# Kernel optimization log

Hardware: AMD Instinct MI355X
Metric: run time of the kernel (lower is better)

The kernel has to match this reference:

```python
import jax, jax.numpy as jnp
import numpy as np

# Quantization constants (from init_kwargs)
INPUT_SCALE = 0.05
OUTPUT_SCALE = 0.1
OUTPUT_ZERO_POINT = 0
FEATURE_BITWIDTH = 8
Q_MIN = -(1 << (FEATURE_BITWIDTH - 1))       # -128
Q_MAX = (1 << (FEATURE_BITWIDTH - 1)) - 1    #  127

B, IN_F, OUT_F = 8192, 4096, 4096


def setup_inputs() -> dict:
    key = jax.random.key(0)
    k_x, k_w, k_b, k_s = jax.random.split(key, 4)
    # int8 quantized activations and weights
    x = jax.random.randint(k_x, (B, IN_F), Q_MIN, Q_MAX + 1, dtype=jnp.int8)
    weight = jax.random.randint(k_w, (OUT_F, IN_F), Q_MIN, Q_MAX + 1, dtype=jnp.int8)
    # shifted quantized bias (int32)
    bias = jax.random.randint(k_b, (OUT_F,), -1000, 1000, dtype=jnp.int32)
    # per-output-channel weight scale (positive floats)
    weight_scale = jax.random.uniform(k_s, (OUT_F,), dtype=jnp.float32, minval=0.001, maxval=0.01)
    return {"x": x, "weight": weight, "bias": bias, "weight_scale": weight_scale}


def reference(x, weight, bias, weight_scale):
    # int32-accumulated GEMM: [B, in] @ [in, out] + bias -> [B, out]
    acc = jnp.matmul(x.astype(jnp.int32), weight.astype(jnp.int32).T,
                     preferred_element_type=jnp.int32) + bias[None, :]
    # dequant/requant epilogue with per-channel scale
    out = acc.astype(jnp.float32) * (INPUT_SCALE * weight_scale[None, :] / OUTPUT_SCALE) + OUTPUT_ZERO_POINT
    out = jnp.clip(jnp.round(out), Q_MIN, Q_MAX).astype(jnp.int8)
    return out
```

## Files before the change

### kernel.cpp

```cpp
#include <hip/hip_runtime.h>
#include <cstdint>
#include <cstddef>

#define M_DIM 8192
#define N_DIM 4096
#define K_DIM 4096

#define BM 128
#define BN 128
#define BK 128

using i32x4 = __attribute__((ext_vector_type(4))) int;

__device__ __forceinline__ void async_load16(const void* g, void* l) {
    __builtin_amdgcn_global_load_lds(
        (const __attribute__((address_space(1))) void*)g,
        (__attribute__((address_space(3))) void*)l,
        16, 0, 0);
}

__global__ __launch_bounds__(256) void pack_i8_fused_kernel(const int4* __restrict__ xsrc,
                                                            const int4* __restrict__ wsrc,
                                                            unsigned* __restrict__ xdst,
                                                            unsigned* __restrict__ wdst,
                                                            long nx4, long ntot4) {
    long i = (long)blockIdx.x * blockDim.x + threadIdx.x;
    if (i >= ntot4) return;
    const int4* src;
    unsigned* dst;
    long si;
    if (i < nx4) { src = xsrc; dst = xdst; si = i; }
    else         { src = wsrc; dst = wdst; si = i - nx4; }
    int4 a = src[si];
    dst[si] = (unsigned)((a.x & 0xff) | ((a.y & 0xff) << 8) |
                         ((a.z & 0xff) << 16) | (a.w << 24));
}

__global__ __launch_bounds__(256) void qgemm_i8_kernel(const int8_t* __restrict__ A,
                                                       const int8_t* __restrict__ B,
                                                       const int* __restrict__ bias,
                                                       const float* __restrict__ wscale,
                                                       int* __restrict__ C) {
    __shared__ int8_t As[2 * BM * 64];
    __shared__ int8_t Bs[2 * BN * 64];

    const int tid  = threadIdx.x;
    const int wave = tid >> 6;
    const int lane = tid & 63;
    const int bm = blockIdx.y;
    const int bn = blockIdx.x;

    const int8_t* Ab = A + (size_t)bm * BM * K_DIM;
    const int8_t* Bb = B + (size_t)bn * BN * K_DIM;

    const int wm = wave >> 1;
    const int wn = wave & 1;

    i32x4 acc[4][4] = {};

    const int rowoff = lane >> 2;
    const int coff   = (lane & 3) * 16;

    const int kq   = (lane >> 4) * 16;
    const int mrow = wm * 64 + (lane & 15);
    const int nrow = wn * 64 + (lane & 15);

    for (int kt = 0; kt < K_DIM; kt += BK) {
#pragma unroll
        for (int c = 0; c < 4; ++c) {
            const int g  = c * 4 + wave;
            const int p  = g >> 3;
            const int rb = g & 7;
            const size_t goff = (size_t)(rb * 16 + rowoff) * K_DIM + kt + p * 64 + coff;
            async_load16(Ab + goff, &As[g * 1024]);
            async_load16(Bb + goff, &Bs[g * 1024]);
        }
        __syncthreads();

#pragma unroll
        for (int p = 0; p < 2; ++p) {
            i32x4 af[4], bf[4];
#pragma unroll
            for (int i = 0; i < 4; ++i)
                af[i] = *(const i32x4*)&As[p * 8192 + (mrow + i * 16) * 64 + kq];
#pragma unroll
            for (int j = 0; j < 4; ++j)
                bf[j] = *(const i32x4*)&Bs[p * 8192 + (nrow + j * 16) * 64 + kq];

#pragma unroll
            for (int i = 0; i < 4; ++i)
#pragma unroll
                for (int j = 0; j < 4; ++j)
                    acc[i][j] = __builtin_amdgcn_mfma_i32_16x16x64_i8(
                        af[i], bf[j], acc[i][j], 0, 0, 0);
        }

        __syncthreads();
    }

    const int col16 = lane & 15;
    const int rquad = (lane >> 4) * 4;
#pragma unroll
    for (int j = 0; j < 4; ++j) {
        const int col = bn * BN + wn * 64 + j * 16 + col16;
        float s = 0.05f * wscale[col];
        s = s / 0.1f;
        const float bz = (float)bias[col];
#pragma unroll
        for (int i = 0; i < 4; ++i) {
            const int row0 = bm * BM + wm * 64 + i * 16 + rquad;
#pragma unroll
            for (int r = 0; r < 4; ++r) {
                float v = ((float)acc[i][j][r] + bz) * s;
                v = rintf(v);
                v = fminf(fmaxf(v, -128.0f), 127.0f);
                C[(size_t)(row0 + r) * N_DIM + col] = (int)v;
            }
        }
    }
}

extern "C" void kernel_launch(void* const* d_in, const int* in_sizes, int n_in,
                              void* d_out, int out_size, void* d_ws, size_t ws_size,
                              hipStream_t stream) {
    const int*   x32    = (const int*)d_in[0];
    const int*   w32    = (const int*)d_in[1];
    const int*   bias   = (const int*)d_in[2];
    const float* wscale = (const float*)d_in[3];
    int*         out    = (int*)d_out;

    int8_t* xp = (int8_t*)d_ws;
    int8_t* wp = xp + (size_t)M_DIM * K_DIM;

    {
        long nx4   = (long)M_DIM * K_DIM / 4;
        long nw4   = (long)N_DIM * K_DIM / 4;
        long ntot4 = nx4 + nw4;
        pack_i8_fused_kernel<<<(int)((ntot4 + 255) / 256), 256, 0, stream>>>(
            (const int4*)x32, (const int4*)w32,
            (unsigned*)xp, (unsigned*)wp, nx4, ntot4);
    }

    dim3 grid(N_DIM / BN, M_DIM / BM);
    qgemm_i8_kernel<<<grid, 256, 0, stream>>>(xp, wp, bias, wscale, out);
}
```

Before: 422.2 us.

## Double-buffer LDS tiles so global loads overlap MFMA compute

Halves the K tile to 64 and splits shared memory into two buffers. Each iteration issues the async global-to-LDS loads for the next K slice before the MFMAs on the current slice run, instead of waiting on each whole tile before computing. The aim is to hide global memory latency behind matrix-core work. LDS size stays the same, but each sync now covers half as much work, and correctness depends on the barrier also waiting for the async LDS writes to finish.

```diff
diff --git a/kernel.cpp b/kernel.cpp
--- a/kernel.cpp
+++ b/kernel.cpp
@@ -8,7 +8,7 @@
 
 #define BM 128
 #define BN 128
-#define BK 128
+#define BK 64
 
 using i32x4 = __attribute__((ext_vector_type(4))) int;
 
@@ -41,8 +41,8 @@
                                                        const int* __restrict__ bias,
                                                        const float* __restrict__ wscale,
                                                        int* __restrict__ C) {
-    __shared__ int8_t As[2 * BM * 64];
-    __shared__ int8_t Bs[2 * BN * 64];
+    __shared__ int8_t As[2][BM * BK];
+    __shared__ int8_t Bs[2][BN * BK];
 
     const int tid  = threadIdx.x;
     const int wave = tid >> 6;
@@ -58,44 +58,50 @@
 
     i32x4 acc[4][4] = {};
 
-    const int rowoff = lane >> 2;
-    const int coff   = (lane & 3) * 16;
+    const int srow = lane >> 2;
+    const int scol = (lane & 3) * 16;
 
     const int kq   = (lane >> 4) * 16;
     const int mrow = wm * 64 + (lane & 15);
     const int nrow = wn * 64 + (lane & 15);
 
-    for (int kt = 0; kt < K_DIM; kt += BK) {
+    auto stage = [&](int kt, int b) {
 #pragma unroll
-        for (int c = 0; c < 4; ++c) {
-            const int g  = c * 4 + wave;
-            const int p  = g >> 3;
-            const int rb = g & 7;
-            const size_t goff = (size_t)(rb * 16 + rowoff) * K_DIM + kt + p * 64 + coff;
-            async_load16(Ab + goff, &As[g * 1024]);
-            async_load16(Bb + goff, &Bs[g * 1024]);
+        for (int c = 0; c < 2; ++c) {
+            const int g = c * 4 + wave;
+            const size_t goff = (size_t)(g * 16 + srow) * K_DIM + kt + scol;
+            async_load16(Ab + goff, &As[b][g * 1024]);
+            async_load16(Bb + goff, &Bs[b][g * 1024]);
         }
-        __syncthreads();
+    };
 
+    auto compute = [&](int b) {
+        i32x4 af[4], bf[4];
 #pragma unroll
-        for (int p = 0; p < 2; ++p) {
-            i32x4 af[4], bf[4];
+        for (int i = 0; i < 4; ++i)
+            af[i] = *(const i32x4*)&As[b][(mrow + i * 16) * BK + kq];
 #pragma unroll
-            for (int i = 0; i < 4; ++i)
-                af[i] = *(const i32x4*)&As[p * 8192 + (mrow + i * 16) * 64 + kq];
+        for (int j = 0; j < 4; ++j)
+            bf[j] = *(const i32x4*)&Bs[b][(nrow + j * 16) * BK + kq];
+#pragma unroll
+        for (int i = 0; i < 4; ++i)
 #pragma unroll
             for (int j = 0; j < 4; ++j)
-                bf[j] = *(const i32x4*)&Bs[p * 8192 + (nrow + j * 16) * 64 + kq];
+                acc[i][j] = __builtin_amdgcn_mfma_i32_16x16x64_i8(
+                    af[i], bf[j], acc[i][j], 0, 0, 0);
+    };
 
-#pragma unroll
-            for (int i = 0; i < 4; ++i)
-#pragma unroll
-                for (int j = 0; j < 4; ++j)
-                    acc[i][j] = __builtin_amdgcn_mfma_i32_16x16x64_i8(
-                        af[i], bf[j], acc[i][j], 0, 0, 0);
-        }
+    stage(0, 0);
+    __syncthreads();
 
+    for (int kt = 0; kt < K_DIM; kt += 2 * BK) {
+        stage(kt + BK, 1);
+        compute(0);
         __syncthreads();
+        const bool more = (kt + 2 * BK) < K_DIM;
+        if (more) stage(kt + 2 * BK, 0);
+        compute(1);
+        if (more) __syncthreads();
     }
 
     const int col16 = lane & 15;
```

Result: slower. 460.7 us (+9.1%).

## Load MFMA fragments directly from global memory with register double-buffering

Applied to the files above, without the earlier changes.

Removes the LDS staging of A and B tiles and the two block-wide barriers per K step. Each wave now reads its MFMA operand fragments straight from global memory into registers, prefetching the next half-step while the current one computes. The cost is that tiles shared by the two waves in a row or column are no longer shared through LDS, so every wave fetches its own copy and the data reuse relies on L1/L2 caches. Each lane also issues scattered 16-byte loads across rows strided by K, which coalesce poorly.

```diff
diff --git a/kernel.cpp b/kernel.cpp
--- a/kernel.cpp
+++ b/kernel.cpp
@@ -6,18 +6,7 @@
 #define N_DIM 4096
 #define K_DIM 4096
 
-#define BM 128
-#define BN 128
-#define BK 128
-
 using i32x4 = __attribute__((ext_vector_type(4))) int;
-
-__device__ __forceinline__ void async_load16(const void* g, void* l) {
-    __builtin_amdgcn_global_load_lds(
-        (const __attribute__((address_space(1))) void*)g,
-        (__attribute__((address_space(3))) void*)l,
-        16, 0, 0);
-}
 
 __global__ __launch_bounds__(256) void pack_i8_fused_kernel(const int4* __restrict__ xsrc,
                                                             const int4* __restrict__ wsrc,
@@ -41,74 +30,62 @@
                                                        const int* __restrict__ bias,
                                                        const float* __restrict__ wscale,
                                                        int* __restrict__ C) {
-    __shared__ int8_t As[2 * BM * 64];
-    __shared__ int8_t Bs[2 * BN * 64];
-
     const int tid  = threadIdx.x;
     const int wave = tid >> 6;
     const int lane = tid & 63;
     const int bm = blockIdx.y;
     const int bn = blockIdx.x;
 
-    const int8_t* Ab = A + (size_t)bm * BM * K_DIM;
-    const int8_t* Bb = B + (size_t)bn * BN * K_DIM;
-
     const int wm = wave >> 1;
     const int wn = wave & 1;
 
+    const int l15 = lane & 15;
+    const int kq  = (lane >> 4) * 16;
+
+    const int8_t* Ap = A + (size_t)(bm * 128 + wm * 64 + l15) * K_DIM + kq;
+    const int8_t* Bp = B + (size_t)(bn * 128 + wn * 64 + l15) * K_DIM + kq;
+
     i32x4 acc[4][4] = {};
+    i32x4 af[2][4], bf[2][4];
 
-    const int rowoff = lane >> 2;
-    const int coff   = (lane & 3) * 16;
+    auto ldfrags = [&](int kt, int s) {
+#pragma unroll
+        for (int i = 0; i < 4; ++i)
+            af[s][i] = *(const i32x4*)(Ap + (size_t)i * (16 * K_DIM) + kt);
+#pragma unroll
+        for (int j = 0; j < 4; ++j)
+            bf[s][j] = *(const i32x4*)(Bp + (size_t)j * (16 * K_DIM) + kt);
+    };
 
-    const int kq   = (lane >> 4) * 16;
-    const int mrow = wm * 64 + (lane & 15);
-    const int nrow = wn * 64 + (lane & 15);
-
-    for (int kt = 0; kt < K_DIM; kt += BK) {
+    auto domfma = [&](int s) {
 #pragma unroll
-        for (int c = 0; c < 4; ++c) {
-            const int g  = c * 4 + wave;
-            const int p  = g >> 3;
-            const int rb = g & 7;
-            const size_t goff = (size_t)(rb * 16 + rowoff) * K_DIM + kt + p * 64 + coff;
-            async_load16(Ab + goff, &As[g * 1024]);
-            async_load16(Bb + goff, &Bs[g * 1024]);
-        }
-        __syncthreads();
-
-#pragma unroll
-        for (int p = 0; p < 2; ++p) {
-            i32x4 af[4], bf[4];
-#pragma unroll
-            for (int i = 0; i < 4; ++i)
-                af[i] = *(const i32x4*)&As[p * 8192 + (mrow + i * 16) * 64 + kq];
+        for (int i = 0; i < 4; ++i)
 #pragma unroll
             for (int j = 0; j < 4; ++j)
-                bf[j] = *(const i32x4*)&Bs[p * 8192 + (nrow + j * 16) * 64 + kq];
+                acc[i][j] = __builtin_amdgcn_mfma_i32_16x16x64_i8(
+                    af[s][i], bf[s][j], acc[i][j], 0, 0, 0);
+    };
 
-#pragma unroll
-            for (int i = 0; i < 4; ++i)
-#pragma unroll
-                for (int j = 0; j < 4; ++j)
-                    acc[i][j] = __builtin_amdgcn_mfma_i32_16x16x64_i8(
-                        af[i], bf[j], acc[i][j], 0, 0, 0);
-        }
-
-        __syncthreads();
+    ldfrags(0, 0);
+    for (int kt = 0; kt < K_DIM; kt += 128) {
+        ldfrags(kt + 64, 1);
+        domfma(0);
+        const int ktn = kt + 128;
+        if (ktn < K_DIM) ldfrags(ktn, 0);
+        domfma(1);
     }
 
     const int col16 = lane & 15;
     const int rquad = (lane >> 4) * 4;
 #pragma unroll
     for (int j = 0; j < 4; ++j) {
-        const int col = bn * BN + wn * 64 + j * 16 + col16;
+        const int col = bn * 128 + wn * 64 + j * 16 + col16;
         float s = 0.05f * wscale[col];
         s = s / 0.1f;
         const float bz = (float)bias[col];
 #pragma unroll
         for (int i = 0; i < 4; ++i) {
-            const int row0 = bm * BM + wm * 64 + i * 16 + rquad;
+            const int row0 = bm * 128 + wm * 64 + i * 16 + rquad;
 #pragma unroll
             for (int r = 0; r < 4; ++r) {
                 float v = ((float)acc[i][j][r] + bz) * s;
@@ -141,6 +118,6 @@
             (unsigned*)xp, (unsigned*)wp, nx4, ntot4);
     }
 
-    dim3 grid(N_DIM / BN, M_DIM / BM);
+    dim3 grid(N_DIM / 128, M_DIM / 128);
     qgemm_i8_kernel<<<grid, 256, 0, stream>>>(xp, wp, bias, wscale, out);
 }
```

New measurement: 708.6 us. 67.8% more time.
